# Kernel optimization log

Hardware: AMD Instinct MI355X
Metric: run time of the kernel (lower is better)

The kernel has to match this reference:

```python
import jax, jax.numpy as jnp
import numpy as np

B, T, F, H = 256, 128, 512, 512

def setup_inputs() -> dict:
    key = jax.random.key(0)
    ks = jax.random.split(key, 6)
    s_in = 1.0 / np.sqrt(F)
    s_rec = 1.0 / np.sqrt(H)
    return {
        "x": jax.random.normal(ks[0], (B, T, F), dtype=jnp.float32),
        "kernel": jax.random.uniform(ks[1], (F, 3 * H), jnp.float32, -s_in, s_in),
        "rec_kernel": jax.random.uniform(ks[2], (H, 3 * H), jnp.float32, -s_rec, s_rec),
        "bias": jnp.zeros((2, 3 * H), dtype=jnp.float32),  # [input_bias, recurrent_bias] (reset_after=True)
        "Wd": jax.random.uniform(ks[3], (H, 1), jnp.float32, -s_rec, s_rec),
        "bd": jnp.zeros((1,), dtype=jnp.float32),
    }

def reference(x, kernel, rec_kernel, bias, Wd, bd):
    # Keras GRU, reset_after=True, activation=relu, recurrent_activation=sigmoid.
    bi, br = bias[0], bias[1]
    # Precompute all input projections: [T, B, 3H]
    xp = jnp.swapaxes(jnp.einsum('btf,fg->btg', x, kernel) + bi, 0, 1)
    h0 = jnp.zeros((x.shape[0], rec_kernel.shape[0]), dtype=x.dtype)

    def step(h, xp_t):
        rec = h @ rec_kernel + br                  # [B, 3H]
        xz, xr, xh = jnp.split(xp_t, 3, axis=-1)
        rz, rr, rh = jnp.split(rec, 3, axis=-1)
        z = jax.nn.sigmoid(xz + rz)                # update gate
        r = jax.nn.sigmoid(xr + rr)                # reset gate
        hh = jax.nn.relu(xh + r * rh)              # candidate (relu activation)
        h_new = z * h + (1.0 - z) * hh
        return h_new, None

    hT, _ = jax.lax.scan(step, h0, xp)
    # Dropout(0.2) is identity at inference. Dense head:
    return hT @ Wd + bd
```

## Files before the change

kernel.cpp:

```cpp
#include <hip/hip_runtime.h>
#include <hip/hip_bf16.h>
#include <math.h>

constexpr int BATCH = 256;
constexpr int SEQ   = 128;
constexpr int FEAT  = 512;
constexpr int HID   = 512;
constexpr int G3    = 1536;

typedef __bf16 bf16x8 __attribute__((ext_vector_type(8)));
typedef float  f32x4  __attribute__((ext_vector_type(4)));
typedef int    i32x4v __attribute__((ext_vector_type(4)));

__global__ __launch_bounds__(256) void convert_bf16(
    const float* __restrict__ in, __hip_bfloat16* __restrict__ out, int n)
{
  int i = (blockIdx.x * 256 + threadIdx.x) * 8;
  if (i >= n) return;
  float4 v0 = *(const float4*)&in[i];
  float4 v1 = *(const float4*)&in[i + 4];
  __hip_bfloat16 o[8];
  o[0] = (__hip_bfloat16)v0.x; o[1] = (__hip_bfloat16)v0.y;
  o[2] = (__hip_bfloat16)v0.z; o[3] = (__hip_bfloat16)v0.w;
  o[4] = (__hip_bfloat16)v1.x; o[5] = (__hip_bfloat16)v1.y;
  o[6] = (__hip_bfloat16)v1.z; o[7] = (__hip_bfloat16)v1.w;
  *(int4*)&out[i] = *(int4*)o;
}

__global__ __launch_bounds__(256) void transpose_convert(
    const float* __restrict__ in, __hip_bfloat16* __restrict__ outT)
{
  __shared__ float tile[32][33];
  const int c0 = blockIdx.x * 32;
  const int r0 = blockIdx.y * 32;
  const int tid = threadIdx.x;
  {
    int row = tid >> 3, c4 = tid & 7;
    float4 v = *(const float4*)&in[(size_t)(r0 + row) * G3 + c0 + c4 * 4];
    tile[row][c4 * 4 + 0] = v.x;
    tile[row][c4 * 4 + 1] = v.y;
    tile[row][c4 * 4 + 2] = v.z;
    tile[row][c4 * 4 + 3] = v.w;
  }
  __syncthreads();
  {
    int rowT = tid >> 3, c4 = tid & 7;
    __hip_bfloat16 o[4];
#pragma unroll
    for (int e = 0; e < 4; ++e)
      o[e] = (__hip_bfloat16)tile[c4 * 4 + e][rowT];
    *(int2*)&outT[(size_t)(c0 + rowT) * FEAT + r0 + c4 * 4] = *(int2*)o;
  }
}

__global__ __launch_bounds__(256) void proj_mfma(
    const __hip_bfloat16* __restrict__ xb, const __hip_bfloat16* __restrict__ WkT,
    const float* __restrict__ bias, __hip_bfloat16* __restrict__ xp)
{
  __shared__ __align__(16) __hip_bfloat16 As[2][128 * 64];
  __shared__ __align__(16) __hip_bfloat16 Bs[2][128 * 64];

  const int tid = threadIdx.x;
  const int wave = tid >> 6, l = tid & 63;
  const int wm = wave >> 1, wn = wave & 1;
  const int m0 = blockIdx.y * 128;
  const int n0 = blockIdx.x * 128;
  const int lr = l & 15, lh = l >> 4;
  const int swz = lr & 7;

  const int srow = l >> 3;
  const int schk = l & 7;
  const int wrow = wave * 32;

  f32x4 acc[4][4] = {};

#define PROJ_STAGE(K0, SEL)                                                      \
  {                                                                              \
    _Pragma("unroll")                                                            \
    for (int i = 0; i < 4; ++i) {                                                \
      int r = wrow + i * 8 + srow;                                               \
      const __hip_bfloat16* srcA =                                               \
          &xb[(size_t)(m0 + r) * FEAT + (K0) + ((schk ^ srow) * 8)];             \
      __builtin_amdgcn_global_load_lds(                                          \
          (const __attribute__((address_space(1))) void*)srcA,                   \
          (__attribute__((address_space(3))) void*)&As[SEL][(wrow + i * 8) * 64],\
          16, 0, 0);                                                             \
    }                                                                            \
    _Pragma("unroll")                                                            \
    for (int i = 0; i < 4; ++i) {                                                \
      int r = wrow + i * 8 + srow;                                               \
      const __hip_bfloat16* srcB =                                               \
          &WkT[(size_t)(n0 + r) * FEAT + (K0) + ((schk ^ srow) * 8)];            \
      __builtin_amdgcn_global_load_lds(                                          \
          (const __attribute__((address_space(1))) void*)srcB,                   \
          (__attribute__((address_space(3))) void*)&Bs[SEL][(wrow + i * 8) * 64],\
          16, 0, 0);                                                             \
    }                                                                            \
  }

  PROJ_STAGE(0, 0);
  __syncthreads();

  int cur = 0;
  for (int kt = 0; kt < 8; ++kt) {
    if (kt < 7) PROJ_STAGE((kt + 1) * 64, cur ^ 1);

#pragma unroll
    for (int ks = 0; ks < 2; ++ks) {
      bf16x8 a[4], b[4];
#pragma unroll
      for (int i = 0; i < 4; ++i) {
        int row = wm * 64 + i * 16 + lr;
        a[i] = *(const bf16x8*)&As[cur][row * 64 + (((ks * 4 + lh) ^ swz) * 8)];
      }
#pragma unroll
      for (int j = 0; j < 4; ++j) {
        int row = wn * 64 + j * 16 + lr;
        b[j] = *(const bf16x8*)&Bs[cur][row * 64 + (((ks * 4 + lh) ^ swz) * 8)];
      }
#pragma unroll
      for (int i = 0; i < 4; ++i)
#pragma unroll
        for (int j = 0; j < 4; ++j)
          acc[i][j] = __builtin_amdgcn_mfma_f32_16x16x32_bf16(a[i], b[j], acc[i][j], 0, 0, 0);
    }
    __syncthreads();
    cur ^= 1;
  }

  float bv[4];
#pragma unroll
  for (int j = 0; j < 4; ++j)
    bv[j] = bias[n0 + wn * 64 + j * 16 + lr];
#pragma unroll
  for (int i = 0; i < 4; ++i)
#pragma unroll
    for (int j = 0; j < 4; ++j) {
      int n = n0 + wn * 64 + j * 16 + lr;
#pragma unroll
      for (int r = 0; r < 4; ++r) {
        int m = m0 + wm * 64 + i * 16 + lh * 4 + r;
        xp[(size_t)m * G3 + n] = (__hip_bfloat16)(acc[i][j][r] + bv[j]);
      }
    }
#undef PROJ_STAGE
}

__global__ __launch_bounds__(256, 1) void gru_persist(
    __hip_bfloat16* __restrict__ hbA, __hip_bfloat16* __restrict__ hbB,
    float* __restrict__ h32,
    const __hip_bfloat16* __restrict__ xp,
    const __hip_bfloat16* __restrict__ WrT,
    const float* __restrict__ br,
    int* slots)
{
  __shared__ float red[2 * 16 * 100];

  const int tid = threadIdx.x;
  const int bt = blockIdx.x & 15;
  const int jt = blockIdx.x >> 4;
  const int wave = tid >> 6, l = tid & 63;
  const int kh = wave & 1, ch = wave >> 1;
  const int lr = l & 15, lh = l >> 4;

  bf16x8 wfrag[8][3];
#pragma unroll
  for (int f = 0; f < 3; ++f) {
    int r = ch * 48 + f * 16 + lr;
    int n = (r >> 5) * HID + jt * 32 + (r & 31);
    const __hip_bfloat16* wp = &WrT[(size_t)n * HID + kh * 256 + lh * 8];
#pragma unroll
    for (int ks = 0; ks < 8; ++ks)
      wfrag[ks][f] = *(const bf16x8*)&wp[ks * 32];
  }
  asm volatile(""
      : "+v"(wfrag[0][0]), "+v"(wfrag[0][1]), "+v"(wfrag[0][2]),
        "+v"(wfrag[1][0]), "+v"(wfrag[1][1]), "+v"(wfrag[1][2]),
        "+v"(wfrag[2][0]), "+v"(wfrag[2][1]), "+v"(wfrag[2][2]),
        "+v"(wfrag[3][0]), "+v"(wfrag[3][1]), "+v"(wfrag[3][2]),
        "+v"(wfrag[4][0]), "+v"(wfrag[4][1]), "+v"(wfrag[4][2]),
        "+v"(wfrag[5][0]), "+v"(wfrag[5][1]), "+v"(wfrag[5][2]),
        "+v"(wfrag[6][0]), "+v"(wfrag[6][1]), "+v"(wfrag[6][2]),
        "+v"(wfrag[7][0]), "+v"(wfrag[7][1]), "+v"(wfrag[7][2]));

  const int m = tid >> 4, q4 = tid & 15;
  const int b = bt * 16 + m;
  const int jl0 = q4 * 2;
  const int jg0 = jt * 32 + jl0;
  float brz[2], brr[2], brh[2], hreg[2];
#pragma unroll
  for (int p = 0; p < 2; ++p) {
    brz[p] = br[jg0 + p];
    brr[p] = br[HID + jg0 + p];
    brh[p] = br[2 * HID + jg0 + p];
    hreg[p] = 0.f;
  }

  float xzv[2], xrv[2], xhv[2];
  {
    const __hip_bfloat16* xb_ = &xp[((size_t)b * SEQ + 0) * G3 + jg0];
    unsigned int uz = *(const unsigned int*)&xb_[0];
    unsigned int ur = *(const unsigned int*)&xb_[HID];
    unsigned int uh = *(const unsigned int*)&xb_[2 * HID];
    xzv[0] = (float)((__hip_bfloat16*)&uz)[0]; xzv[1] = (float)((__hip_bfloat16*)&uz)[1];
    xrv[0] = (float)((__hip_bfloat16*)&ur)[0]; xrv[1] = (float)((__hip_bfloat16*)&ur)[1];
    xhv[0] = (float)((__hip_bfloat16*)&uh)[0]; xhv[1] = (float)((__hip_bfloat16*)&uh)[1];
  }

  const char* baseA = (const char*)hbA + ((size_t)(bt * 16 + lr) * HID + kh * 256 + lh * 8) * 2;
  const char* baseB = (const char*)hbB + ((size_t)(bt * 16 + lr) * HID + kh * 256 + lh * 8) * 2;

  for (int t = 0; t < SEQ; ++t) {
    const char* hp = (t & 1) ? baseB : baseA;
    __hip_bfloat16* nxt = (t & 1) ? hbA : hbB;

    i32x4v r0, r1, r2, r3, r4, r5, r6, r7;
    asm volatile(
        "global_load_dwordx4 %0, %8, off sc0 sc1\n\t"
        "global_load_dwordx4 %1, %8, off offset:64 sc0 sc1\n\t"
        "global_load_dwordx4 %2, %8, off offset:128 sc0 sc1\n\t"
        "global_load_dwordx4 %3, %8, off offset:192 sc0 sc1\n\t"
        "global_load_dwordx4 %4, %8, off offset:256 sc0 sc1\n\t"
        "global_load_dwordx4 %5, %8, off offset:320 sc0 sc1\n\t"
        "global_load_dwordx4 %6, %8, off offset:384 sc0 sc1\n\t"
        "global_load_dwordx4 %7, %8, off offset:448 sc0 sc1\n\t"
        "s_waitcnt vmcnt(0)"
        : "=&v"(r0), "=&v"(r1), "=&v"(r2), "=&v"(r3),
          "=&v"(r4), "=&v"(r5), "=&v"(r6), "=&v"(r7)
        : "v"(hp)
        : "memory");
    union { i32x4v q; bf16x8 v; } u0, u1, u2, u3, u4, u5, u6, u7;
    u0.q = r0; u1.q = r1; u2.q = r2; u3.q = r3;
    u4.q = r4; u5.q = r5; u6.q = r6; u7.q = r7;
    bf16x8 afrag[8] = {u0.v, u1.v, u2.v, u3.v, u4.v, u5.v, u6.v, u7.v};

    f32x4 acc[3] = {};
#pragma unroll
    for (int ks = 0; ks < 8; ++ks)
#pragma unroll
      for (int f = 0; f < 3; ++f)
        acc[f] = __builtin_amdgcn_mfma_f32_16x16x32_bf16(afrag[ks], wfrag[ks][f], acc[f], 0, 0, 0);

#pragma unroll
    for (int f = 0; f < 3; ++f)
#pragma unroll
      for (int i = 0; i < 4; ++i)
        red[kh * 1600 + (lh * 4 + i) * 100 + ch * 48 + f * 16 + lr] = acc[f][i];
    __syncthreads();

    {
      float hn[2];
#pragma unroll
      for (int p = 0; p < 2; ++p) {
        int jl = jl0 + p;
        float rz = red[m * 100 + jl]      + red[1600 + m * 100 + jl];
        float rr = red[m * 100 + 32 + jl] + red[1600 + m * 100 + 32 + jl];
        float rh = red[m * 100 + 64 + jl] + red[1600 + m * 100 + 64 + jl];
        rz += brz[p]; rr += brr[p]; rh += brh[p];
        float z  = 1.f / (1.f + __expf(-(xzv[p] + rz)));
        float rg = 1.f / (1.f + __expf(-(xrv[p] + rr)));
        float hh = fmaxf(xhv[p] + rg * rh, 0.f);
        hn[p] = z * hreg[p] + (1.f - z) * hh;
        hreg[p] = hn[p];
      }
      if (t < SEQ - 1) {
        __hip_bfloat16 h0 = (__hip_bfloat16)hn[0], h1 = (__hip_bfloat16)hn[1];
        unsigned int pk = (unsigned int)*(unsigned short*)&h0 |
                          ((unsigned int)*(unsigned short*)&h1 << 16);
        __hip_atomic_store(
            (unsigned int*)&nxt[(size_t)b * HID + jg0], pk,
            __ATOMIC_RELAXED, __HIP_MEMORY_SCOPE_AGENT);

        const __hip_bfloat16* xb_ = &xp[((size_t)b * SEQ + t + 1) * G3 + jg0];
        unsigned int uz = *(const unsigned int*)&xb_[0];
        unsigned int ur = *(const unsigned int*)&xb_[HID];
        unsigned int uh = *(const unsigned int*)&xb_[2 * HID];
        xzv[0] = (float)((__hip_bfloat16*)&uz)[0]; xzv[1] = (float)((__hip_bfloat16*)&uz)[1];
        xrv[0] = (float)((__hip_bfloat16*)&ur)[0]; xrv[1] = (float)((__hip_bfloat16*)&ur)[1];
        xhv[0] = (float)((__hip_bfloat16*)&uh)[0]; xhv[1] = (float)((__hip_bfloat16*)&uh)[1];
      }
    }

    if (t < SEQ - 1) {
      __syncthreads();
      if (tid == 0) {
        __hip_atomic_store(&slots[bt * 32 + jt], t + 1,
                           __ATOMIC_RELAXED, __HIP_MEMORY_SCOPE_AGENT);
        const char* fl = (const char*)&slots[bt * 32];
        for (;;) {
          i32x4v p0, p1, p2, p3;
          asm volatile(
              "global_load_dwordx4 %0, %4, off sc0 sc1\n\t"
              "global_load_dwordx4 %1, %4, off offset:16 sc0 sc1\n\t"
              "global_load_dwordx4 %2, %4, off offset:32 sc0 sc1\n\t"
              "global_load_dwordx4 %3, %4, off offset:48 sc0 sc1\n\t"
              "s_waitcnt vmcnt(0)"
              : "=&v"(p0), "=&v"(p1), "=&v"(p2), "=&v"(p3)
              : "v"(fl)
              : "memory");
          int t1 = t + 1;
          int ok = (p0[0] >= t1) & (p0[1] >= t1) & (p0[2] >= t1) & (p0[3] >= t1) &
                   (p1[0] >= t1) & (p1[1] >= t1) & (p1[2] >= t1) & (p1[3] >= t1) &
                   (p2[0] >= t1) & (p2[1] >= t1) & (p2[2] >= t1) & (p2[3] >= t1) &
                   (p3[0] >= t1) & (p3[1] >= t1) & (p3[2] >= t1) & (p3[3] >= t1);
          if (ok) break;
          __builtin_amdgcn_s_sleep(1);
        }
      }
      __syncthreads();
    }
  }

#pragma unroll
  for (int p = 0; p < 2; ++p)
    h32[(size_t)b * HID + jg0 + p] = hreg[p];
}

__global__ __launch_bounds__(64) void head_kernel(
    const float* __restrict__ h32, const float* __restrict__ Wd,
    const float* __restrict__ bd, float* __restrict__ out)
{
  int b = blockIdx.x, l = threadIdx.x;
  const float* hr = &h32[(size_t)b * HID];
  float s = 0.f;
#pragma unroll
  for (int i = 0; i < 8; ++i)
    s += hr[l + i * 64] * Wd[l + i * 64];
#pragma unroll
  for (int off = 32; off; off >>= 1) s += __shfl_down(s, off);
  if (l == 0) out[b] = s + bd[0];
}

extern "C" void kernel_launch(void* const* d_in, const int* in_sizes, int n_in,
                              void* d_out, int out_size, void* d_ws, size_t ws_size,
                              hipStream_t stream) {
  const float* x    = (const float*)d_in[0];
  const float* Wk   = (const float*)d_in[1];
  const float* Wr   = (const float*)d_in[2];
  const float* bias = (const float*)d_in[3];
  const float* Wd   = (const float*)d_in[4];
  const float* bd   = (const float*)d_in[5];
  float* out = (float*)d_out;

  char* ws = (char*)d_ws;
  size_t off = 0;
  __hip_bfloat16* xp  = (__hip_bfloat16*)(ws + off); off += (size_t)BATCH * SEQ * G3 * 2;
  __hip_bfloat16* xb  = (__hip_bfloat16*)(ws + off); off += (size_t)BATCH * SEQ * FEAT * 2;
  __hip_bfloat16* WkT = (__hip_bfloat16*)(ws + off); off += (size_t)G3 * FEAT * 2;
  __hip_bfloat16* WrT = (__hip_bfloat16*)(ws + off); off += (size_t)G3 * HID * 2;
  float*          h32 = (float*)(ws + off);          off += (size_t)BATCH * HID * 4;
  __hip_bfloat16* hb0 = (__hip_bfloat16*)(ws + off); off += (size_t)BATCH * HID * 2;
  __hip_bfloat16* hb1 = (__hip_bfloat16*)(ws + off); off += (size_t)BATCH * HID * 2;
  int*            slots = (int*)(ws + off);          off += 16 * 32 * sizeof(int);

  convert_bf16<<<(BATCH * SEQ * FEAT) / (256 * 8), 256, 0, stream>>>(x, xb, BATCH * SEQ * FEAT);
  transpose_convert<<<dim3(G3 / 32, FEAT / 32), 256, 0, stream>>>(Wk, WkT);
  transpose_convert<<<dim3(G3 / 32, HID  / 32), 256, 0, stream>>>(Wr, WrT);

  proj_mfma<<<dim3(G3 / 128, (BATCH * SEQ) / 128), 256, 0, stream>>>(xb, WkT, bias, xp);

  hipMemsetAsync(hb0, 0, (size_t)BATCH * HID * sizeof(__hip_bfloat16), stream);
  hipMemsetAsync(slots, 0, 16 * 32 * sizeof(int), stream);

  const float* br = bias + G3;
  {
    void* args[] = {(void*)&hb0, (void*)&hb1, (void*)&h32, (void*)&xp,
                    (void*)&WrT, (void*)&br, (void*)&slots};
    hipLaunchCooperativeKernel((void*)gru_persist, dim3(256), dim3(256),
                               args, 0, stream);
  }

  head_kernel<<<256, 64, 0, stream>>>(h32, Wd, bd, out);
}
```

Measured before the change: 453.9 us.

## Replace pre-publish block barrier with LDS wave counter and tighten step loop

In the persistent GRU kernel, the block-wide __syncthreads before publishing the step flag is removed. Instead, each wave waits for its own stores to drain (vmcnt(0)) and bumps a workgroup-scope LDS counter, and the last wave to arrive publishes the flag. The per-step xp loads now sit at the top of each step, so they overlap the h-state loads, and the s_sleep in the spin-wait is removed to cut wake-up latency. The slot array is compacted to 16 entries per batch tile. The risks are correctness of the relaxed-ordering publish and more polling traffic from the tighter spin.

```diff
diff --git a/kernel.cpp b/kernel.cpp
--- a/kernel.cpp
+++ b/kernel.cpp
@@ -155,6 +155,7 @@
     int* slots)
 {
   __shared__ float red[2 * 16 * 100];
+  __shared__ int wdone;
 
   const int tid = threadIdx.x;
   const int bt = blockIdx.x & 15;
@@ -196,16 +197,7 @@
     hreg[p] = 0.f;
   }
 
-  float xzv[2], xrv[2], xhv[2];
-  {
-    const __hip_bfloat16* xb_ = &xp[((size_t)b * SEQ + 0) * G3 + jg0];
-    unsigned int uz = *(const unsigned int*)&xb_[0];
-    unsigned int ur = *(const unsigned int*)&xb_[HID];
-    unsigned int uh = *(const unsigned int*)&xb_[2 * HID];
-    xzv[0] = (float)((__hip_bfloat16*)&uz)[0]; xzv[1] = (float)((__hip_bfloat16*)&uz)[1];
-    xrv[0] = (float)((__hip_bfloat16*)&ur)[0]; xrv[1] = (float)((__hip_bfloat16*)&ur)[1];
-    xhv[0] = (float)((__hip_bfloat16*)&uh)[0]; xhv[1] = (float)((__hip_bfloat16*)&uh)[1];
-  }
+  if (tid == 0) wdone = 0;
 
   const char* baseA = (const char*)hbA + ((size_t)(bt * 16 + lr) * HID + kh * 256 + lh * 8) * 2;
   const char* baseB = (const char*)hbB + ((size_t)(bt * 16 + lr) * HID + kh * 256 + lh * 8) * 2;
@@ -213,6 +205,11 @@
   for (int t = 0; t < SEQ; ++t) {
     const char* hp = (t & 1) ? baseB : baseA;
     __hip_bfloat16* nxt = (t & 1) ? hbA : hbB;
+
+    const __hip_bfloat16* xq = &xp[((size_t)b * SEQ + t) * G3 + jg0];
+    unsigned int uz = *(const unsigned int*)&xq[0];
+    unsigned int ur_ = *(const unsigned int*)&xq[HID];
+    unsigned int uh_ = *(const unsigned int*)&xq[2 * HID];
 
     i32x4v r0, r1, r2, r3, r4, r5, r6, r7;
     asm volatile(
@@ -249,6 +246,10 @@
     __syncthreads();
 
     {
+      float xzv[2], xrv[2], xhv[2];
+      xzv[0] = (float)((__hip_bfloat16*)&uz)[0];  xzv[1] = (float)((__hip_bfloat16*)&uz)[1];
+      xrv[0] = (float)((__hip_bfloat16*)&ur_)[0]; xrv[1] = (float)((__hip_bfloat16*)&ur_)[1];
+      xhv[0] = (float)((__hip_bfloat16*)&uh_)[0]; xhv[1] = (float)((__hip_bfloat16*)&uh_)[1];
       float hn[2];
 #pragma unroll
       for (int p = 0; p < 2; ++p) {
@@ -270,23 +271,21 @@
         __hip_atomic_store(
             (unsigned int*)&nxt[(size_t)b * HID + jg0], pk,
             __ATOMIC_RELAXED, __HIP_MEMORY_SCOPE_AGENT);
-
-        const __hip_bfloat16* xb_ = &xp[((size_t)b * SEQ + t + 1) * G3 + jg0];
-        unsigned int uz = *(const unsigned int*)&xb_[0];
-        unsigned int ur = *(const unsigned int*)&xb_[HID];
-        unsigned int uh = *(const unsigned int*)&xb_[2 * HID];
-        xzv[0] = (float)((__hip_bfloat16*)&uz)[0]; xzv[1] = (float)((__hip_bfloat16*)&uz)[1];
-        xrv[0] = (float)((__hip_bfloat16*)&ur)[0]; xrv[1] = (float)((__hip_bfloat16*)&ur)[1];
-        xhv[0] = (float)((__hip_bfloat16*)&uh)[0]; xhv[1] = (float)((__hip_bfloat16*)&uh)[1];
       }
     }
 
     if (t < SEQ - 1) {
-      __syncthreads();
+      asm volatile("s_waitcnt vmcnt(0)" ::: "memory");
+      if (l == 0) {
+        int old = __hip_atomic_fetch_add(&wdone, 1, __ATOMIC_RELAXED,
+                                         __HIP_MEMORY_SCOPE_WORKGROUP);
+        if (old == 4 * t + 3) {
+          __hip_atomic_store(&slots[bt * 16 + jt], t + 1,
+                             __ATOMIC_RELAXED, __HIP_MEMORY_SCOPE_AGENT);
+        }
+      }
       if (tid == 0) {
-        __hip_atomic_store(&slots[bt * 32 + jt], t + 1,
-                           __ATOMIC_RELAXED, __HIP_MEMORY_SCOPE_AGENT);
-        const char* fl = (const char*)&slots[bt * 32];
+        const char* fl = (const char*)&slots[bt * 16];
         for (;;) {
           i32x4v p0, p1, p2, p3;
           asm volatile(
@@ -304,7 +303,6 @@
                    (p2[0] >= t1) & (p2[1] >= t1) & (p2[2] >= t1) & (p2[3] >= t1) &
                    (p3[0] >= t1) & (p3[1] >= t1) & (p3[2] >= t1) & (p3[3] >= t1);
           if (ok) break;
-          __builtin_amdgcn_s_sleep(1);
         }
       }
       __syncthreads();
@@ -351,7 +349,7 @@
   float*          h32 = (float*)(ws + off);          off += (size_t)BATCH * HID * 4;
   __hip_bfloat16* hb0 = (__hip_bfloat16*)(ws + off); off += (size_t)BATCH * HID * 2;
   __hip_bfloat16* hb1 = (__hip_bfloat16*)(ws + off); off += (size_t)BATCH * HID * 2;
-  int*            slots = (int*)(ws + off);          off += 16 * 32 * sizeof(int);
+  int*            slots = (int*)(ws + off);          off += 16 * 16 * sizeof(int);
 
   convert_bf16<<<(BATCH * SEQ * FEAT) / (256 * 8), 256, 0, stream>>>(x, xb, BATCH * SEQ * FEAT);
   transpose_convert<<<dim3(G3 / 32, FEAT / 32), 256, 0, stream>>>(Wk, WkT);
@@ -360,7 +358,7 @@
   proj_mfma<<<dim3(G3 / 128, (BATCH * SEQ) / 128), 256, 0, stream>>>(xb, WkT, bias, xp);
 
   hipMemsetAsync(hb0, 0, (size_t)BATCH * HID * sizeof(__hip_bfloat16), stream);
-  hipMemsetAsync(slots, 0, 16 * 32 * sizeof(int), stream);
+  hipMemsetAsync(slots, 0, 16 * 16 * sizeof(int), stream);
 
   const float* br = bias + G3;
   {
```

Measured after the change: 712.0 us. 1.57x slower.
